# Performance work log

Hardware: AMD Instinct MI355X
Metric: run time of the kernel (lower is better)

## Reference

```python
import jax, jax.numpy as jnp
import numpy as np

B, S, E, H = 2, 2048, 2048, 16
D = E // H          # head_dim = 128
RD = 128            # rotary_emb_dim (== head_dim here)
BASE = 10000.0


def setup_inputs() -> dict:
    key = jax.random.key(0)
    k1, k2, k3, k4, k5 = jax.random.split(key, 5)
    scale = 0.02
    return {
        "x": jax.random.normal(k1, (B, S, E), dtype=jnp.float32),
        "wqkv_w": jax.random.normal(k2, (3 * E, E), dtype=jnp.float32) * scale,
        "wqkv_b": jax.random.normal(k3, (3 * E,), dtype=jnp.float32) * scale,
        "out_w": jax.random.normal(k4, (E, E), dtype=jnp.float32) * scale,
        "out_b": jax.random.normal(k5, (E,), dtype=jnp.float32) * scale,
    }


def _rope_cos_sin(seqlen, dtype):
    inv_freq = 1.0 / (BASE ** (jnp.arange(0, RD, 2, dtype=jnp.float32) / RD))
    t = jnp.arange(seqlen, dtype=jnp.float32)
    freqs = jnp.outer(t, inv_freq)          # (S, RD//2)
    return jnp.cos(freqs).astype(dtype), jnp.sin(freqs).astype(dtype)


def _apply_rotary(v, cos, sin):
    # v: (B, S, H, D); rotate first RD dims (here RD == D)
    v_rot, v_pass = v[..., :RD], v[..., RD:]
    v1, v2 = jnp.split(v_rot, 2, axis=-1)    # each (B, S, H, RD//2)
    c = cos[None, :, None, :]
    s = sin[None, :, None, :]
    rot = jnp.concatenate([v1 * c - v2 * s, v1 * s + v2 * c], axis=-1)
    return jnp.concatenate([rot, v_pass], axis=-1)


def reference(x, wqkv_w, wqkv_b, out_w, out_b):
    b, s, e = x.shape
    # column-parallel QKV projection (world size 1)
    qkv = jnp.einsum("bse,fe->bsf", x, wqkv_w) + wqkv_b     # (B, S, 3E)
    qkv = qkv.reshape(b, s, 3, H, D)
    cos, sin = _rope_cos_sin(s, x.dtype)
    q = _apply_rotary(qkv[:, :, 0], cos, sin)               # (B, S, H, D)
    k = _apply_rotary(qkv[:, :, 1], cos, sin)
    v = qkv[:, :, 2]
    # causal self-attention, softmax_scale = 1/sqrt(head_dim)
    scale = 1.0 / jnp.sqrt(jnp.asarray(D, dtype=x.dtype))
    scores = jnp.einsum("bshd,bthd->bhst", q, k) * scale    # (B, H, S, S)
    causal_mask = jnp.tril(jnp.ones((s, s), dtype=bool))
    scores = jnp.where(causal_mask[None, None], scores, jnp.finfo(x.dtype).min)
    probs = jax.nn.softmax(scores, axis=-1)
    ctx = jnp.einsum("bhst,bthd->bshd", probs, v)           # (B, S, H, D)
    # row-parallel output projection
    out = jnp.einsum("bse,fe->bsf", ctx.reshape(b, s, e), out_w) + out_b
    return out
```

## Files before the change

### kernel.cpp

```cpp
#include <hip/hip_runtime.h>
#include <cstdint>
#include <cstddef>

#define Bd 2
#define Sd 2048
#define Ed 2048
#define Hd 16
#define Dd 128
#define N3E 6144
#define ATT_SCALE 0.08838834764831845f

typedef short bf16x8 __attribute__((ext_vector_type(8)));
typedef float f32x4 __attribute__((ext_vector_type(4)));
typedef float f32x16 __attribute__((ext_vector_type(16)));

__device__ __forceinline__ float bf2f(unsigned short u) {
    union { unsigned int u; float f; } c;
    c.u = ((unsigned int)u) << 16;
    return c.f;
}
__device__ __forceinline__ unsigned short f2bf(float f) {
    union { float f; unsigned int u; } c;
    c.f = f;
    unsigned int x = c.u;
    x += 0x7FFFu + ((x >> 16) & 1u);
    return (unsigned short)(x >> 16);
}

__device__ __forceinline__ void gl2lds16(const void* g, void* l) {
    __builtin_amdgcn_global_load_lds(
        (const __attribute__((address_space(1))) void*)g,
        (__attribute__((address_space(3))) void*)l, 16, 0, 0);
}

__global__ void cvt_all(const float* __restrict__ x,
                        const float* __restrict__ w1,
                        const float* __restrict__ w2,
                        unsigned short* __restrict__ ox,
                        unsigned short* __restrict__ o1,
                        unsigned short* __restrict__ o2) {
    int i = (blockIdx.x * 256 + threadIdx.x) * 4;
    const float* s;
    unsigned short* d;
    int off;
    if (i < 8388608) { s = x; d = ox; off = i; }
    else if (i < 20971520) { s = w1; d = o1; off = i - 8388608; }
    else { s = w2; d = o2; off = i - 20971520; }
    const float4 v = *(const float4*)(s + off);
    d[off + 0] = f2bf(v.x);
    d[off + 1] = f2bf(v.y);
    d[off + 2] = f2bf(v.z);
    d[off + 3] = f2bf(v.w);
}

template <int MODE>
__global__ void gemm_bt(const unsigned short* __restrict__ A,
                        const unsigned short* __restrict__ Bm,
                        const float* __restrict__ bias,
                        void* __restrict__ o0, void* __restrict__ o1,
                        void* __restrict__ o2, int Ndim, int K) {
    __shared__ __align__(16) unsigned short U[16640];
    unsigned short* As = U;
    unsigned short* Bs = U + 8192;

    const int tid = threadIdx.x;
    const int lane = tid & 63;
    const int wave = tid >> 6;
    const int quad = lane >> 4;
    const int l16 = lane & 15;
    const int wr = wave >> 1;
    const int wc = wave & 1;

    const int n0 = blockIdx.x * 128;
    const int m0 = blockIdx.y * 128;

    const unsigned short* Ab = A + (size_t)m0 * K;
    const unsigned short* Bb = Bm + (size_t)n0 * K;

    const f32x4 fzero = {0.f, 0.f, 0.f, 0.f};
    f32x4 acc[4][4];
#pragma unroll
    for (int i = 0; i < 4; i++)
#pragma unroll
        for (int j = 0; j < 4; j++) acc[i][j] = fzero;

    for (int k0 = 0; k0 < K; k0 += 64) {
        __syncthreads();
#pragma unroll
        for (int it = 0; it < 4; ++it) {
            int L = it * 256 + tid;
            int row = L >> 3;
            int cs = L & 7;
            int gc = cs ^ (row & 7);
            gl2lds16(Ab + row * K + k0 + gc * 8, (void*)(As + L * 8));
            gl2lds16(Bb + row * K + k0 + gc * 8, (void*)(Bs + L * 8));
        }
        __syncthreads();
#pragma unroll
        for (int kk = 0; kk < 2; ++kk) {
            bf16x8 af[4], bfr[4];
#pragma unroll
            for (int i = 0; i < 4; i++) {
                int row = wr * 64 + i * 16 + l16;
                int cs = kk * 4 + quad;
                af[i] = *(const bf16x8*)(As + row * 64 + (cs ^ (row & 7)) * 8);
            }
#pragma unroll
            for (int j = 0; j < 4; j++) {
                int row = wc * 64 + j * 16 + l16;
                int cs = kk * 4 + quad;
                bfr[j] = *(const bf16x8*)(Bs + row * 64 + (cs ^ (row & 7)) * 8);
            }
#pragma unroll
            for (int i = 0; i < 4; i++)
#pragma unroll
                for (int j = 0; j < 4; j++)
                    acc[i][j] = __builtin_amdgcn_mfma_f32_16x16x32_bf16(
                        af[i], bfr[j], acc[i][j], 0, 0, 0);
        }
    }

    if (MODE == 0) {
#pragma unroll
        for (int j = 0; j < 4; j++) {
            int col = n0 + wc * 64 + j * 16 + l16;
            float bv = bias[col];
#pragma unroll
            for (int i = 0; i < 4; i++) {
                int rbase = m0 + wr * 64 + i * 16 + quad * 4;
#pragma unroll
                for (int r = 0; r < 4; r++)
                    ((float*)o0)[(size_t)(rbase + r) * Ndim + col] =
                        acc[i][j][r] + bv;
            }
        }
    } else {
        __syncthreads();
#pragma unroll
        for (int j = 0; j < 4; j++) {
            int coll = wc * 64 + j * 16 + l16;
            float bv = bias[n0 + coll];
#pragma unroll
            for (int i = 0; i < 4; i++) {
                int rl = wr * 64 + i * 16 + quad * 4;
#pragma unroll
                for (int r = 0; r < 4; r++)
                    U[(rl + r) * 130 + coll] = f2bf(acc[i][j][r] + bv);
            }
        }
        __syncthreads();

        const int ch = n0 >> 7;
        const int c = ch >> 4;
        const int h = ch & 15;
        const int bb = m0 >> 11;
        const int s0 = m0 & 2047;

        if (c < 2) {
            unsigned short* dstq = (unsigned short*)(c == 0 ? o0 : o1);
            const size_t hb = ((size_t)(bb * Hd + h)) * Sd;
#pragma unroll
            for (int it = 0; it < 16; ++it) {
                int lin = it * 256 + tid;
                int row = lin >> 5, p = lin & 31;
                int s = s0 + row;
                unsigned int lo = *(const unsigned int*)(U + row * 130 + 2 * p);
                unsigned int hi =
                    *(const unsigned int*)(U + row * 130 + 64 + 2 * p);
                float v1a = bf2f((unsigned short)lo), v1b = bf2f(lo >> 16);
                float v2a = bf2f((unsigned short)hi), v2b = bf2f(hi >> 16);
                float fa = (float)s * __expf(-(float)(2 * p) *
                                             (9.210340371976184f / 64.0f));
                float fb = (float)s * __expf(-(float)(2 * p + 1) *
                                             (9.210340371976184f / 64.0f));
                float sna, csa, snb, csb;
                __sincosf(fa, &sna, &csa);
                __sincosf(fb, &snb, &csb);
                ushort2 r1, r2;
                r1.x = f2bf(v1a * csa - v2a * sna);
                r1.y = f2bf(v1b * csb - v2b * snb);
                r2.x = f2bf(v1a * sna + v2a * csa);
                r2.y = f2bf(v1b * snb + v2b * csb);
                unsigned short* dst = dstq + (hb + s) * Dd;
                *(ushort2*)(dst + 2 * p) = r1;
                *(ushort2*)(dst + 64 + 2 * p) = r2;
            }
        } else {
            unsigned short* dstv = (unsigned short*)o2;
            const size_t hb = ((size_t)(bb * Hd + h)) * Dd;
#pragma unroll
            for (int it = 0; it < 16; ++it) {
                int lin = it * 256 + tid;
                int d = lin >> 5, sc = lin & 31;
                int s4 = sc * 4;
                ushort4 pk;
                pk.x = U[(s4 + 0) * 130 + d];
                pk.y = U[(s4 + 1) * 130 + d];
                pk.z = U[(s4 + 2) * 130 + d];
                pk.w = U[(s4 + 3) * 130 + d];
                *(ushort4*)(dstv + (hb + d) * Sd + s0 + s4) = pk;
            }
        }
    }
}

__global__ __launch_bounds__(256, 2) void flash_attn(
    const unsigned short* __restrict__ q, const unsigned short* __restrict__ k,
    const unsigned short* __restrict__ vt, unsigned short* __restrict__ ctx) {
    __shared__ __align__(16) unsigned short Ks[2][64 * 128];
    __shared__ __align__(16) unsigned short Vts[2][128 * 64];
    __shared__ __align__(16) unsigned short Ps[128 * 64];

    const int tid = threadIdx.x;
    const int lane = tid & 63;
    const int wave = tid >> 6;
    const int l32 = lane & 31;
    const int half = lane >> 5;

    const int yy = blockIdx.y;
    const int qi = (yy < 8) ? 15 - yy : yy - 8;
    const int bh = blockIdx.x;
    const int q0 = qi * 128;
    const int qg = q0 + wave * 32 + l32;
    const int prow = wave * 32 + l32;
    const int psw = prow & 7;

    const unsigned short* kb = k + (size_t)bh * Sd * Dd;
    const unsigned short* vtb = vt + (size_t)bh * Dd * Sd;

    bf16x8 aq[8];
    {
        const unsigned short* qrow = q + ((size_t)bh * Sd + qg) * Dd;
#pragma unroll
        for (int ks = 0; ks < 8; ks++)
            aq[ks] = *(const bf16x8*)(qrow + ks * 16 + half * 8);
    }

    f32x16 o[4];
#pragma unroll
    for (int db = 0; db < 4; db++)
#pragma unroll
        for (int r = 0; r < 16; r++) o[db][r] = 0.f;
    float mi = -3.0e38f, li = 0.f;

    auto stage = [&](int b, int t0) {
#pragma unroll
        for (int it = 0; it < 4; ++it) {
            int L = it * 256 + tid;
            int rk = L >> 4;
            int ck = L & 15;
            int gk = ck ^ (rk & 15);
            gl2lds16(kb + (size_t)(t0 + rk) * Dd + gk * 8,
                     (void*)(&Ks[b][0] + L * 8));
            int rv = L >> 3;
            int cv = L & 7;
            int gv = cv ^ (rv & 7);
            gl2lds16(vtb + (size_t)rv * Sd + t0 + gv * 8,
                     (void*)(&Vts[b][0] + L * 8));
        }
    };

    const int tmax = q0 + 64;
    stage(0, 0);
    int cur = 0;
    for (int t0 = 0; t0 <= tmax; t0 += 64) {
        __syncthreads();
        if (t0 + 64 <= tmax) stage(cur ^ 1, t0 + 64);
        const unsigned short* Ksc = &Ks[cur][0];
        const unsigned short* Vtsc = &Vts[cur][0];

        f32x16 sa[2];
#pragma unroll
        for (int b2 = 0; b2 < 2; b2++)
#pragma unroll
            for (int r = 0; r < 16; r++) sa[b2][r] = 0.f;
#pragma unroll
        for (int ks = 0; ks < 8; ks++) {
            int cd = ks * 2 + half;
#pragma unroll
            for (int b2 = 0; b2 < 2; b2++) {
                int row = b2 * 32 + l32;
                bf16x8 ak = *(const bf16x8*)(Ksc + row * 128 +
                                             (cd ^ (row & 15)) * 8);
                sa[b2] = __builtin_amdgcn_mfma_f32_32x32x16_bf16(ak, aq[ks],
                                                                 sa[b2], 0, 0, 0);
            }
        }

        float mx = -3.0e38f;
#pragma unroll
        for (int b2 = 0; b2 < 2; b2++)
#pragma unroll
            for (int r = 0; r < 16; r++) {
                float v = sa[b2][r] * ATT_SCALE;
                int tg = t0 + b2 * 32 + (r & 3) + 8 * (r >> 2) + 4 * half;
                if (tg > qg) v = -3.0e38f;
                sa[b2][r] = v;
                mx = fmaxf(mx, v);
            }
        mx = fmaxf(mx, __shfl_xor(mx, 32, 64));
        const float mnew = fmaxf(mi, mx);
        const float alpha = __expf(mi - mnew);
        float rs = 0.f;
#pragma unroll
        for (int b2 = 0; b2 < 2; b2++)
#pragma unroll
            for (int r = 0; r < 16; r++) {
                float pp = __expf(sa[b2][r] - mnew);
                sa[b2][r] = pp;
                rs += pp;
            }
        rs += __shfl_xor(rs, 32, 64);
        li = li * alpha + rs;
        mi = mnew;

#pragma unroll
        for (int db = 0; db < 4; db++)
#pragma unroll
            for (int r = 0; r < 16; r++) o[db][r] *= alpha;

#pragma unroll
        for (int b2 = 0; b2 < 2; b2++)
#pragma unroll
            for (int g = 0; g < 4; g++) {
                ushort4 pk;
                pk.x = f2bf(sa[b2][g * 4 + 0]);
                pk.y = f2bf(sa[b2][g * 4 + 1]);
                pk.z = f2bf(sa[b2][g * 4 + 2]);
                pk.w = f2bf(sa[b2][g * 4 + 3]);
                *(ushort4*)(Ps + prow * 64 + ((b2 * 4 + g) ^ psw) * 8 +
                            half * 4) = pk;
            }

#pragma unroll
        for (int kk = 0; kk < 4; kk++) {
            bf16x8 bp = *(const bf16x8*)(Ps + prow * 64 +
                                         ((kk * 2 + half) ^ psw) * 8);
#pragma unroll
            for (int db = 0; db < 4; db++) {
                int row = db * 32 + l32;
                bf16x8 av = *(const bf16x8*)(
                    Vtsc + row * 64 + ((kk * 2 + half) ^ (row & 7)) * 8);
                o[db] = __builtin_amdgcn_mfma_f32_32x32x16_bf16(av, bp, o[db],
                                                                0, 0, 0);
            }
        }
        cur ^= 1;
    }

    const int b = bh >> 4;
    const int h = bh & 15;
    const float inv = 1.0f / li;
    unsigned short* dst = ctx + ((size_t)(b * Sd + qg)) * Ed + h * Dd;
#pragma unroll
    for (int db = 0; db < 4; db++)
#pragma unroll
        for (int g = 0; g < 4; g++) {
            ushort4 pk;
            pk.x = f2bf(o[db][g * 4 + 0] * inv);
            pk.y = f2bf(o[db][g * 4 + 1] * inv);
            pk.z = f2bf(o[db][g * 4 + 2] * inv);
            pk.w = f2bf(o[db][g * 4 + 3] * inv);
            *(ushort4*)(dst + db * 32 + g * 8 + half * 4) = pk;
        }
}

extern "C" void kernel_launch(void* const* d_in, const int* in_sizes, int n_in,
                              void* d_out, int out_size, void* d_ws,
                              size_t ws_size, hipStream_t stream) {
    const float* x = (const float*)d_in[0];
    const float* wqkv_w = (const float*)d_in[1];
    const float* wqkv_b = (const float*)d_in[2];
    const float* out_w = (const float*)d_in[3];
    const float* out_b = (const float*)d_in[4];
    float* out = (float*)d_out;

    char* ws = (char*)d_ws;
    unsigned short* xb    = (unsigned short*)(ws + 0);
    unsigned short* wqkvb = (unsigned short*)(ws + 16777216);
    unsigned short* owb   = (unsigned short*)(ws + 41943040);
    unsigned short* qb    = (unsigned short*)(ws + 50331648);
    unsigned short* kb    = (unsigned short*)(ws + 67108864);
    unsigned short* vtb   = (unsigned short*)(ws + 83886080);
    unsigned short* ctx   = (unsigned short*)(ws + 0);

    cvt_all<<<24576, 256, 0, stream>>>(x, wqkv_w, out_w, xb, wqkvb, owb);
    gemm_bt<1><<<dim3(48, 32), 256, 0, stream>>>(xb, wqkvb, wqkv_b, qb, kb, vtb,
                                                 N3E, Ed);
    flash_attn<<<dim3(32, 16), 256, 0, stream>>>(qb, kb, vtb, ctx);
    gemm_bt<0><<<dim3(16, 32), 256, 0, stream>>>(ctx, owb, out_b, out, nullptr,
                                                 nullptr, Ed, Ed);
}
```

Before: 345.1 us.

## Skip fully-masked tiles per wave and use lazy-rescale exp2 softmax

Each wave skips the QK/PV work for key tiles lying entirely above its causal diagonal, and applies the causal mask only on diagonal tiles. Softmax moves to base-2 with the log2e factor folded into the scale, and uses the raw v_exp_f32 instruction. The running max is rescaled only when it grows by more than 11 (in log2 units), which removes most per-tile multiplies of the accumulator. bf16 packing now uses the hardware v_cvt_pk_bf16_f32. The lazy rescale allows unnormalised values up to about 2^11 in fp32 and bf16, a bounded precision tradeoff.

```diff
diff --git a/kernel.cpp b/kernel.cpp
--- a/kernel.cpp
+++ b/kernel.cpp
@@ -9,6 +9,7 @@
 #define Dd 128
 #define N3E 6144
 #define ATT_SCALE 0.08838834764831845f
+#define C2LOG 0.12751743f
 
 typedef short bf16x8 __attribute__((ext_vector_type(8)));
 typedef float f32x4 __attribute__((ext_vector_type(4)));
@@ -25,6 +26,17 @@
     unsigned int x = c.u;
     x += 0x7FFFu + ((x >> 16) & 1u);
     return (unsigned short)(x >> 16);
+}
+
+__device__ __forceinline__ float exp2_fast(float x) {
+    float r;
+    asm("v_exp_f32 %0, %1" : "=v"(r) : "v"(x));
+    return r;
+}
+__device__ __forceinline__ unsigned int cvtpk_bf16(float lo, float hi) {
+    unsigned int r;
+    asm("v_cvt_pk_bf16_f32 %0, %1, %2" : "=v"(r) : "v"(lo), "v"(hi));
+    return r;
 }
 
 __device__ __forceinline__ void gl2lds16(const void* g, void* l) {
@@ -266,83 +278,94 @@
     for (int t0 = 0; t0 <= tmax; t0 += 64) {
         __syncthreads();
         if (t0 + 64 <= tmax) stage(cur ^ 1, t0 + 64);
-        const unsigned short* Ksc = &Ks[cur][0];
-        const unsigned short* Vtsc = &Vts[cur][0];
-
-        f32x16 sa[2];
-#pragma unroll
-        for (int b2 = 0; b2 < 2; b2++)
-#pragma unroll
-            for (int r = 0; r < 16; r++) sa[b2][r] = 0.f;
-#pragma unroll
-        for (int ks = 0; ks < 8; ks++) {
-            int cd = ks * 2 + half;
-#pragma unroll
-            for (int b2 = 0; b2 < 2; b2++) {
-                int row = b2 * 32 + l32;
-                bf16x8 ak = *(const bf16x8*)(Ksc + row * 128 +
-                                             (cd ^ (row & 15)) * 8);
-                sa[b2] = __builtin_amdgcn_mfma_f32_32x32x16_bf16(ak, aq[ks],
-                                                                 sa[b2], 0, 0, 0);
-            }
-        }
-
-        float mx = -3.0e38f;
-#pragma unroll
-        for (int b2 = 0; b2 < 2; b2++)
-#pragma unroll
-            for (int r = 0; r < 16; r++) {
-                float v = sa[b2][r] * ATT_SCALE;
-                int tg = t0 + b2 * 32 + (r & 3) + 8 * (r >> 2) + 4 * half;
-                if (tg > qg) v = -3.0e38f;
-                sa[b2][r] = v;
-                mx = fmaxf(mx, v);
-            }
-        mx = fmaxf(mx, __shfl_xor(mx, 32, 64));
-        const float mnew = fmaxf(mi, mx);
-        const float alpha = __expf(mi - mnew);
-        float rs = 0.f;
-#pragma unroll
-        for (int b2 = 0; b2 < 2; b2++)
-#pragma unroll
-            for (int r = 0; r < 16; r++) {
-                float pp = __expf(sa[b2][r] - mnew);
-                sa[b2][r] = pp;
-                rs += pp;
-            }
-        rs += __shfl_xor(rs, 32, 64);
-        li = li * alpha + rs;
-        mi = mnew;
-
-#pragma unroll
-        for (int db = 0; db < 4; db++)
-#pragma unroll
-            for (int r = 0; r < 16; r++) o[db][r] *= alpha;
-
-#pragma unroll
-        for (int b2 = 0; b2 < 2; b2++)
-#pragma unroll
-            for (int g = 0; g < 4; g++) {
-                ushort4 pk;
-                pk.x = f2bf(sa[b2][g * 4 + 0]);
-                pk.y = f2bf(sa[b2][g * 4 + 1]);
-                pk.z = f2bf(sa[b2][g * 4 + 2]);
-                pk.w = f2bf(sa[b2][g * 4 + 3]);
-                *(ushort4*)(Ps + prow * 64 + ((b2 * 4 + g) ^ psw) * 8 +
-                            half * 4) = pk;
-            }
-
-#pragma unroll
-        for (int kk = 0; kk < 4; kk++) {
-            bf16x8 bp = *(const bf16x8*)(Ps + prow * 64 +
-                                         ((kk * 2 + half) ^ psw) * 8);
-#pragma unroll
-            for (int db = 0; db < 4; db++) {
-                int row = db * 32 + l32;
-                bf16x8 av = *(const bf16x8*)(
-                    Vtsc + row * 64 + ((kk * 2 + half) ^ (row & 7)) * 8);
-                o[db] = __builtin_amdgcn_mfma_f32_32x32x16_bf16(av, bp, o[db],
-                                                                0, 0, 0);
+
+        if (t0 <= q0 + wave * 32 + 31) {
+            const unsigned short* Ksc = &Ks[cur][0];
+            const unsigned short* Vtsc = &Vts[cur][0];
+
+            f32x16 sa[2];
+#pragma unroll
+            for (int b2 = 0; b2 < 2; b2++)
+#pragma unroll
+                for (int r = 0; r < 16; r++) sa[b2][r] = 0.f;
+#pragma unroll
+            for (int ks = 0; ks < 8; ks++) {
+                int cd = ks * 2 + half;
+#pragma unroll
+                for (int b2 = 0; b2 < 2; b2++) {
+                    int row = b2 * 32 + l32;
+                    bf16x8 ak = *(const bf16x8*)(Ksc + row * 128 +
+                                                 (cd ^ (row & 15)) * 8);
+                    sa[b2] = __builtin_amdgcn_mfma_f32_32x32x16_bf16(
+                        ak, aq[ks], sa[b2], 0, 0, 0);
+                }
+            }
+
+            float mx = -3.0e38f;
+            if (t0 + 63 > q0 + wave * 32) {
+#pragma unroll
+                for (int b2 = 0; b2 < 2; b2++)
+#pragma unroll
+                    for (int r = 0; r < 16; r++) {
+                        float v = sa[b2][r] * C2LOG;
+                        int tg = t0 + b2 * 32 + (r & 3) + 8 * (r >> 2) + 4 * half;
+                        if (tg > qg) v = -3.0e38f;
+                        sa[b2][r] = v;
+                        mx = fmaxf(mx, v);
+                    }
+            } else {
+#pragma unroll
+                for (int b2 = 0; b2 < 2; b2++)
+#pragma unroll
+                    for (int r = 0; r < 16; r++) {
+                        float v = sa[b2][r] * C2LOG;
+                        sa[b2][r] = v;
+                        mx = fmaxf(mx, v);
+                    }
+            }
+            mx = fmaxf(mx, __shfl_xor(mx, 32, 64));
+
+            if (mx > mi + 11.0f) {
+                const float al = exp2_fast(mi - mx);
+                mi = mx;
+                li *= al;
+#pragma unroll
+                for (int db = 0; db < 4; db++)
+#pragma unroll
+                    for (int r = 0; r < 16; r++) o[db][r] *= al;
+            }
+
+            float rs = 0.f;
+#pragma unroll
+            for (int b2 = 0; b2 < 2; b2++)
+#pragma unroll
+                for (int g = 0; g < 4; g++) {
+                    float p0 = exp2_fast(sa[b2][g * 4 + 0] - mi);
+                    float p1 = exp2_fast(sa[b2][g * 4 + 1] - mi);
+                    float p2 = exp2_fast(sa[b2][g * 4 + 2] - mi);
+                    float p3 = exp2_fast(sa[b2][g * 4 + 3] - mi);
+                    rs += (p0 + p1) + (p2 + p3);
+                    uint2 w;
+                    w.x = cvtpk_bf16(p0, p1);
+                    w.y = cvtpk_bf16(p2, p3);
+                    *(uint2*)(Ps + prow * 64 + ((b2 * 4 + g) ^ psw) * 8 +
+                              half * 4) = w;
+                }
+            rs += __shfl_xor(rs, 32, 64);
+            li += rs;
+
+#pragma unroll
+            for (int kk = 0; kk < 4; kk++) {
+                bf16x8 bp = *(const bf16x8*)(Ps + prow * 64 +
+                                             ((kk * 2 + half) ^ psw) * 8);
+#pragma unroll
+                for (int db = 0; db < 4; db++) {
+                    int row = db * 32 + l32;
+                    bf16x8 av = *(const bf16x8*)(
+                        Vtsc + row * 64 + ((kk * 2 + half) ^ (row & 7)) * 8);
+                    o[db] = __builtin_amdgcn_mfma_f32_32x32x16_bf16(
+                        av, bp, o[db], 0, 0, 0);
+                }
             }
         }
         cur ^= 1;
@@ -356,12 +379,10 @@
     for (int db = 0; db < 4; db++)
 #pragma unroll
         for (int g = 0; g < 4; g++) {
-            ushort4 pk;
-            pk.x = f2bf(o[db][g * 4 + 0] * inv);
-            pk.y = f2bf(o[db][g * 4 + 1] * inv);
-            pk.z = f2bf(o[db][g * 4 + 2] * inv);
-            pk.w = f2bf(o[db][g * 4 + 3] * inv);
-            *(ushort4*)(dst + db * 32 + g * 8 + half * 4) = pk;
+            uint2 w;
+            w.x = cvtpk_bf16(o[db][g * 4 + 0] * inv, o[db][g * 4 + 1] * inv);
+            w.y = cvtpk_bf16(o[db][g * 4 + 2] * inv, o[db][g * 4 + 3] * inv);
+            *(uint2*)(dst + db * 32 + g * 8 + half * 4) = w;
         }
 }
 
```

After: 345.5 us (median of 2 runs). Within noise of the previous version (+0.1%).
